# Kernel tuning notes

Measured on AMD Instinct MI355X. Metric: run time of the kernel, lower is better.

## Reference

```python
import jax, jax.numpy as jnp
import numpy as np

B, N, DIM = 4, 1024, 512
H, DH = 8, 64
INNER = H * DH
MLP = 2048
EPS = 1e-5


def layernorm(x, g, b):
    m = x.mean(-1, keepdims=True)
    v = ((x - m) ** 2).mean(-1, keepdims=True)
    return (x - m) / jnp.sqrt(v + EPS) * g + b


def setup_inputs() -> dict:
    key = jax.random.key(0)
    ks = jax.random.split(key, 12)
    s = 0.02
    return {
        "q": jax.random.normal(ks[0], (B, N, DIM), jnp.float32),
        "k": jax.random.normal(ks[1], (B, N, DIM), jnp.float32),
        "v": jax.random.normal(ks[2], (B, N, DIM), jnp.float32),
        "Win": jax.random.normal(ks[3], (INNER, DIM), jnp.float32) * s,
        "Wout": jax.random.normal(ks[4], (DIM, INNER), jnp.float32) * s,
        "bout": jnp.zeros((DIM,), jnp.float32),
        "g1": jnp.ones((DIM,), jnp.float32),
        "b1n": jnp.zeros((DIM,), jnp.float32),
        "g2": jnp.ones((DIM,), jnp.float32),
        "b2n": jnp.zeros((DIM,), jnp.float32),
        "Wup": jax.random.normal(ks[5], (MLP, DIM), jnp.float32) * s,
        "bup": jnp.zeros((MLP,), jnp.float32),
        "Wdn": jax.random.normal(ks[6], (DIM, MLP), jnp.float32) * s,
        "bdn": jnp.zeros((DIM,), jnp.float32),
        "wp_W1": jax.random.normal(ks[7], (DH, 2 * DH), jnp.float32) * s,
        "wp_b1": jnp.zeros((DH,), jnp.float32),
        "wp_g": jnp.ones((DH,), jnp.float32),
        "wp_b": jnp.zeros((DH,), jnp.float32),
        "wp_W2": jax.random.normal(ks[8], (3, DH), jnp.float32) * s,
        "wp_b2": jnp.zeros((3,), jnp.float32),
        "num_heads": H,
        "dim_head": DH,
        "mlp_dim": MLP,
    }


def reference(q, k, v, Win, Wout, bout, g1, b1n, g2, b2n, Wup, bup, Wdn, bdn,
              wp_W1, wp_b1, wp_g, wp_b, wp_W2, wp_b2, num_heads, dim_head, mlp_dim):
    b, n, _ = q.shape

    def split_heads(x):  # [b,n,dim] -> [h,b,n,d]
        f = x @ Win.T
        return f.reshape(b, n, num_heads, dim_head).transpose(2, 0, 1, 3)

    fq = split_heads(layernorm(q, g1, b1n))
    fk = split_heads(layernorm(k, g1, b1n))
    fv = split_heads(layernorm(v, g1, b1n))

    # cosine similarity component
    dots = jnp.einsum('hbnd,hbmd->hbnm', fq, fk)
    nq = jnp.linalg.norm(fq, axis=-1)  # [h,b,n]
    nk = jnp.linalg.norm(fk, axis=-1)  # [h,b,m]
    cosine_sim = dots / (nq[..., :, None] * nk[..., None, :])

    # mean-centered covariance component
    qc = fq - fq.mean(-1, keepdims=True)
    kc = fk - fk.mean(-1, keepdims=True)
    cov_component = jnp.einsum('hbnd,hbmd->hbnm', qc, kc) / dim_head

    # variance outer-product component (torch.var -> unbiased, ddof=1)
    qv = jnp.var(fq, axis=-1, ddof=1)  # [h,b,n]
    kv = jnp.var(fk, axis=-1, ddof=1)  # [h,b,m]
    var_component = qv[..., :, None] * kv[..., None, :] / dim_head

    # dynamic per-head mixing weights
    qg = fq.mean(axis=(1, 2))  # [h,d]
    kg = fk.mean(axis=(1, 2))
    feats = jnp.concatenate([qg, kg], axis=-1)  # [h,2d]
    h1 = jax.nn.relu(layernorm(feats @ wp_W1.T + wp_b1, wp_g, wp_b))
    w = jax.nn.softmax(h1 @ wp_W2.T + wp_b2, axis=-1)  # [h,3]
    cw = w[:, 0][:, None, None, None]
    covw = w[:, 1][:, None, None, None]
    vw = w[:, 2][:, None, None, None]

    scores = cw * cosine_sim + covw * cov_component + vw * var_component
    out = jnp.einsum('hbnm,hbmd->hbnd', scores, fv)
    out = out.transpose(1, 2, 0, 3).reshape(b, n, num_heads * dim_head)
    attn = out @ Wout.T + bout

    q2 = q + attn
    x = layernorm(q2, g2, b2n)
    y = jax.nn.gelu(x @ Wup.T + bup, approximate=False) @ Wdn.T + bdn
    return q2 + y
```

## Files before the change

kernel.cpp:

```cpp
#include <hip/hip_runtime.h>
#include <math.h>

#define EPS 1e-5f
#define ROWS 4096

typedef __attribute__((ext_vector_type(8))) short short8;
typedef __attribute__((ext_vector_type(4))) float floatx4;

__device__ inline short f2bf(float f) {
    unsigned u = __builtin_bit_cast(unsigned, f);
    unsigned r = (u + 0x7fffu + ((u >> 16) & 1u)) >> 16;
    return (short)r;
}
__device__ inline float bf2f(short s) {
    return __builtin_bit_cast(float, (unsigned)(unsigned short)s << 16);
}

__global__ __launch_bounds__(256) void prep(
    const float* __restrict__ q, const float* __restrict__ k,
    const float* __restrict__ v, const float* __restrict__ g,
    const float* __restrict__ bb, short* __restrict__ qkvout,
    const float* __restrict__ w0, const float* __restrict__ w1,
    const float* __restrict__ w2, const float* __restrict__ w3,
    short* __restrict__ o0, short* __restrict__ o1,
    short* __restrict__ o2, short* __restrict__ o3,
    const float* __restrict__ g2, const float* __restrict__ b2n,
    float* __restrict__ Bn, float* __restrict__ Wg,
    float* __restrict__ zero0) {
    int bx = blockIdx.x;
    int t = threadIdx.x;
    if (bx < 3072) {
        int tensor = bx >> 10;
        int xb = bx & 1023;
        const float* x = tensor == 0 ? q : (tensor == 1 ? k : v);
        int row = xb * 4 + (t >> 6);
        int col = (t & 63) * 8;
        const float* xr = x + (size_t)row * 512 + col;
        float4 v0 = *(const float4*)xr;
        float4 v1 = *(const float4*)(xr + 4);
        float s = v0.x + v0.y + v0.z + v0.w + v1.x + v1.y + v1.z + v1.w;
        float sq = v0.x * v0.x + v0.y * v0.y + v0.z * v0.z + v0.w * v0.w +
                   v1.x * v1.x + v1.y * v1.y + v1.z * v1.z + v1.w * v1.w;
#pragma unroll
        for (int off = 32; off; off >>= 1) {
            s += __shfl_xor(s, off);
            sq += __shfl_xor(sq, off);
        }
        float m = s * (1.f / 512.f);
        float rstd = rsqrtf(sq * (1.f / 512.f) - m * m + EPS);
        float4 g0 = *(const float4*)(g + col);
        float4 g1 = *(const float4*)(g + col + 4);
        float4 b0 = *(const float4*)(bb + col);
        float4 b1 = *(const float4*)(bb + col + 4);
        short8 o;
        o[0] = f2bf((v0.x - m) * rstd * g0.x + b0.x);
        o[1] = f2bf((v0.y - m) * rstd * g0.y + b0.y);
        o[2] = f2bf((v0.z - m) * rstd * g0.z + b0.z);
        o[3] = f2bf((v0.w - m) * rstd * g0.w + b0.w);
        o[4] = f2bf((v1.x - m) * rstd * g1.x + b1.x);
        o[5] = f2bf((v1.y - m) * rstd * g1.y + b1.y);
        o[6] = f2bf((v1.z - m) * rstd * g1.z + b1.z);
        o[7] = f2bf((v1.w - m) * rstd * g1.w + b1.w);
        *(short8*)(qkvout + (size_t)(tensor * 4096 + row) * 512 + col) = o;
        return;
    }
    if (bx < 4352) {
        int wb = bx - 3072;
        if (wb >= 256 && wb < 768) {
            int base = wb - 256;
            int idx = base * 2048 + t * 8;
            int n = idx >> 9, c = idx & 511;
            float4 v0 = *(const float4*)(w2 + idx);
            float4 v1 = *(const float4*)(w2 + idx + 4);
            float4 ga = *(const float4*)(g2 + c);
            float4 gb = *(const float4*)(g2 + c + 4);
            float4 ba = *(const float4*)(b2n + c);
            float4 bbv = *(const float4*)(b2n + c + 4);
            short8 o;
            o[0] = f2bf(ga.x * v0.x); o[1] = f2bf(ga.y * v0.y);
            o[2] = f2bf(ga.z * v0.z); o[3] = f2bf(ga.w * v0.w);
            o[4] = f2bf(gb.x * v1.x); o[5] = f2bf(gb.y * v1.y);
            o[6] = f2bf(gb.z * v1.z); o[7] = f2bf(gb.w * v1.w);
            *(short8*)(o2 + idx) = o;
            float bn = ba.x * v0.x + ba.y * v0.y + ba.z * v0.z + ba.w * v0.w +
                       bbv.x * v1.x + bbv.y * v1.y + bbv.z * v1.z + bbv.w * v1.w;
            float wg = ga.x * v0.x + ga.y * v0.y + ga.z * v0.z + ga.w * v0.w +
                       gb.x * v1.x + gb.y * v1.y + gb.z * v1.z + gb.w * v1.w;
#pragma unroll
            for (int off = 32; off; off >>= 1) {
                bn += __shfl_xor(bn, off);
                wg += __shfl_xor(wg, off);
            }
            if ((t & 63) == 0) {
                Bn[n] = bn;
                Wg[n] = wg;
            }
            return;
        }
        const float* src;
        short* dst;
        int base;
        if (wb < 128) { src = w0; dst = o0; base = wb; }
        else if (wb < 256) { src = w1; dst = o1; base = wb - 128; }
        else { src = w3; dst = o3; base = wb - 768; }
        int idx = base * 2048 + t * 8;
        float4 v0 = *(const float4*)(src + idx);
        float4 v1 = *(const float4*)(src + idx + 4);
        short8 o;
        o[0] = f2bf(v0.x); o[1] = f2bf(v0.y); o[2] = f2bf(v0.z); o[3] = f2bf(v0.w);
        o[4] = f2bf(v1.x); o[5] = f2bf(v1.y); o[6] = f2bf(v1.z); o[7] = f2bf(v1.w);
        *(short8*)(dst + idx) = o;
        return;
    }
    int zi = (bx - 4352) * 1024 + t * 4;
    if (zi < 275456) *(float4*)(zero0 + zi) = (float4){0.f, 0.f, 0.f, 0.f};
}

template <int TM, int TN, int EPI, bool OUT_BF16>
__global__ __launch_bounds__(256) void mfma_gemm_nt(
    const short* __restrict__ A, const short* __restrict__ B,
    void* __restrict__ C, int M, int N, int K, int ldk,
    const float* __restrict__ bias, const float* __restrict__ resid,
    short* __restrict__ C2, float* __restrict__ Sb,
    float* __restrict__ qgp, float* __restrict__ kgp) {
    constexpr int FI = TM / 32;
    constexpr int FJ = TN / 32;
    __shared__ short As[2][TM * 32];
    __shared__ short Bs[2][TN * 32];
    int t = threadIdx.x;
    int m0 = blockIdx.y * TM, n0 = blockIdx.x * TN;
    int w = t >> 6, lane = t & 63;
    int wm = (w & 1) * (TM / 2), wn = (w >> 1) * (TN / 2);
    floatx4 acc[FI][FJ];
#pragma unroll
    for (int i = 0; i < FI; ++i)
#pragma unroll
        for (int j = 0; j < FJ; ++j) acc[i][j] = (floatx4){0.f, 0.f, 0.f, 0.f};

    int arow = t >> 2, acol = (t & 3) * 8;
    const short* Ag = A + (size_t)(m0 + arow) * ldk + acol;
    const short* Bg = B + (size_t)(n0 + arow) * ldk + acol;
    int ldsbase = w * 1024;

    auto stage = [&](int k0, int buf) {
#pragma unroll
        for (int u = 0; u < TM / 64; ++u)
            __builtin_amdgcn_global_load_lds(
                (const __attribute__((address_space(1))) void*)(Ag + (size_t)u * 64 * ldk + k0),
                (__attribute__((address_space(3))) void*)((char*)As[buf] + u * 4096 + ldsbase),
                16, 0, 0);
#pragma unroll
        for (int u = 0; u < TN / 64; ++u)
            __builtin_amdgcn_global_load_lds(
                (const __attribute__((address_space(1))) void*)(Bg + (size_t)u * 64 * ldk + k0),
                (__attribute__((address_space(3))) void*)((char*)Bs[buf] + u * 4096 + ldsbase),
                16, 0, 0);
    };

    stage(0, 0);
    __syncthreads();
    int nsteps = K >> 5;
    for (int ks = 0; ks < nsteps; ++ks) {
        int buf = ks & 1;
        if (ks + 1 < nsteps) stage((ks + 1) << 5, buf ^ 1);
        int krow = (lane >> 4) * 8;
        short8 af[FI], bf[FJ];
#pragma unroll
        for (int i = 0; i < FI; ++i)
            af[i] = *(const short8*)&As[buf][(wm + i * 16 + (lane & 15)) * 32 + krow];
#pragma unroll
        for (int j = 0; j < FJ; ++j)
            bf[j] = *(const short8*)&Bs[buf][(wn + j * 16 + (lane & 15)) * 32 + krow];
#pragma unroll
        for (int i = 0; i < FI; ++i)
#pragma unroll
            for (int j = 0; j < FJ; ++j)
                acc[i][j] = __builtin_amdgcn_mfma_f32_16x16x32_bf16(
                    af[i], bf[j], acc[i][j], 0, 0, 0);
        __syncthreads();
    }

    int col = lane & 15, rbase = (lane >> 4) * 4;
    if constexpr (EPI == 5) {
#pragma unroll
        for (int i = 0; i < FI; ++i) {
#pragma unroll
            for (int r = 0; r < 4; ++r) {
                int grow = m0 + wm + i * 16 + rbase + r;
                float s = 0.f, sq = 0.f;
#pragma unroll
                for (int j = 0; j < FJ; ++j) {
                    int gcol = n0 + wn + j * 16 + col;
                    float vv = acc[i][j][r] + bias[gcol] +
                               resid[(size_t)grow * N + gcol];
                    ((float*)C)[(size_t)grow * N + gcol] = vv;
                    C2[(size_t)grow * N + gcol] = f2bf(vv);
                    s += vv;
                    sq += vv * vv;
                }
#pragma unroll
                for (int off = 1; off < 16; off <<= 1) {
                    s += __shfl_xor(s, off);
                    sq += __shfl_xor(sq, off);
                }
                if ((lane & 15) == 0) {
                    atomicAdd(&Sb[grow], s);
                    atomicAdd(&Sb[4096 + grow], sq);
                }
            }
        }
    } else if constexpr (EPI == 4) {
#pragma unroll
        for (int i = 0; i < FI; ++i) {
#pragma unroll
            for (int r = 0; r < 4; ++r) {
                int grow = m0 + wm + i * 16 + rbase + r;
                float m = Sb[grow] * (1.f / 512.f);
                float rstd = rsqrtf(Sb[4096 + grow] * (1.f / 512.f) - m * m + EPS);
                float mrstd = m * rstd;
#pragma unroll
                for (int j = 0; j < FJ; ++j) {
                    int gcol = n0 + wn + j * 16 + col;
                    float vv = rstd * acc[i][j][r] + qgp[gcol] + bias[gcol] -
                               mrstd * kgp[gcol];
                    vv = 0.5f * vv * (1.f + erff(vv * 0.70710678118654752f));
                    ((short*)C)[(size_t)grow * N + gcol] = f2bf(vv);
                }
            }
        }
    } else {
#pragma unroll
        for (int i = 0; i < FI; ++i) {
#pragma unroll
            for (int j = 0; j < FJ; ++j) {
                int gcol = n0 + wn + j * 16 + col;
#pragma unroll
                for (int r = 0; r < 4; ++r) {
                    int grow = m0 + wm + i * 16 + rbase + r;
                    float v = acc[i][j][r];
                    if (EPI == 2) v += bias[gcol] + resid[(size_t)grow * N + gcol];
                    if (OUT_BF16)
                        ((short*)C)[(size_t)grow * N + gcol] = f2bf(v);
                    else
                        ((float*)C)[(size_t)grow * N + gcol] = v;
                }
            }
        }
    }

    if constexpr (EPI == 1) {
        if (m0 < 8192) {
            int tensor = m0 >> 12;
            float* Sbase = Sb + (size_t)tensor * 98304;
            float* dst = tensor ? kgp : qgp;
            int head = (n0 + wn) >> 6;
            int rowbase = (m0 & 4095) + wm;
#pragma unroll
            for (int i = 0; i < FI; ++i) {
#pragma unroll
                for (int r = 0; r < 4; ++r) {
                    float s = 0.f, sq = 0.f;
#pragma unroll
                    for (int j = 0; j < FJ; ++j) {
                        float vv = acc[i][j][r];
                        s += vv;
                        sq += vv * vv;
                    }
#pragma unroll
                    for (int off = 1; off < 16; off <<= 1) {
                        s += __shfl_xor(s, off);
                        sq += __shfl_xor(sq, off);
                    }
                    if ((lane & 15) == 0) {
                        int row = rowbase + i * 16 + rbase + r;
                        int idx = head * ROWS + row;
                        float m = s * (1.f / 64.f);
                        Sbase[idx] = m;
                        Sbase[32768 + idx] = rsqrtf(sq);
                        Sbase[65536 + idx] = (sq - 64.f * m * m) * (1.f / 63.f);
                    }
                }
            }
            float cs[FJ];
#pragma unroll
            for (int j = 0; j < FJ; ++j) {
                float s = 0.f;
#pragma unroll
                for (int i = 0; i < FI; ++i)
#pragma unroll
                    for (int r = 0; r < 4; ++r) s += acc[i][j][r];
                s += __shfl_xor(s, 16);
                s += __shfl_xor(s, 32);
                cs[j] = s;
            }
            if (lane < 16) {
#pragma unroll
                for (int j = 0; j < FJ; ++j)
                    atomicAdd(&dst[head * 64 + j * 16 + lane], cs[j] * (1.f / 4096.f));
            }
        }
    }
}

__global__ __launch_bounds__(256) void kside_fused(
    const short* __restrict__ fkb, const short* __restrict__ fvb,
    const float* __restrict__ rnk, const float* __restrict__ kvv,
    const float* __restrict__ mkm, float* __restrict__ Mnew,
    float* __restrict__ Sv,
    const float* __restrict__ qg, const float* __restrict__ kg,
    const float* __restrict__ W1, const float* __restrict__ b1,
    const float* __restrict__ g, const float* __restrict__ bb,
    const float* __restrict__ W2, const float* __restrict__ b2,
    float* __restrict__ wmix) {
    int t = threadIdx.x;
    if (blockIdx.x == 32) {
        int wv = t >> 6;
        if (wv >= 2) return;
        int h = blockIdx.y * 2 + wv;
        int j = t & 63;
        float acc = 0.f;
        const float* w1r = W1 + j * 128;
        for (int i = 0; i < 64; ++i) acc += qg[h * 64 + i] * w1r[i];
        for (int i = 0; i < 64; ++i) acc += kg[h * 64 + i] * w1r[64 + i];
        acc += b1[j];
        float s = acc, sq = acc * acc;
#pragma unroll
        for (int off = 32; off; off >>= 1) {
            s += __shfl_xor(s, off);
            sq += __shfl_xor(sq, off);
        }
        float m = s * (1.f / 64.f);
        float var = sq * (1.f / 64.f) - m * m;
        float xh = (acc - m) * rsqrtf(var + EPS) * g[j] + bb[j];
        float r = fmaxf(xh, 0.f);
        float l[3];
#pragma unroll
        for (int c = 0; c < 3; ++c) {
            float p = r * W2[c * 64 + j];
#pragma unroll
            for (int off = 32; off; off >>= 1) p += __shfl_xor(p, off);
            l[c] = p + b2[c];
        }
        if (j == 0) {
            float mx = fmaxf(l[0], fmaxf(l[1], l[2]));
            float e0 = expf(l[0] - mx), e1 = expf(l[1] - mx), e2 = expf(l[2] - mx);
            float inv = 1.f / (e0 + e1 + e2);
            wmix[h * 3 + 0] = e0 * inv;
            wmix[h * 3 + 1] = e1 * inv;
            wmix[h * 3 + 2] = e2 * inv;
        }
        return;
    }
    int hb = blockIdx.x, kz = blockIdx.y;
    int h = hb >> 2, b = hb & 3;
    __shared__ __attribute__((aligned(16))) short rawK[32 * 72];
    __shared__ __attribute__((aligned(16))) short rawV[32 * 72];
    __shared__ __attribute__((aligned(16))) short Ktp[64 * 40];
    __shared__ __attribute__((aligned(16))) short Ktr[64 * 40];
    __shared__ __attribute__((aligned(16))) short Vt[64 * 40];
    __shared__ float rs[256], kvs[256], mks[256];
    {
        int sidx = h * ROWS + b * 1024 + kz * 256 + t;
        rs[t] = rnk[sidx];
        kvs[t] = kvv[sidx];
        mks[t] = mkm[sidx];
    }
    int w = t >> 6, lane = t & 63;
    int wm = (w & 1) * 32, wn = (w >> 1) * 32;
    floatx4 accP[2][2], accR[2][2];
#pragma unroll
    for (int i = 0; i < 2; ++i)
#pragma unroll
        for (int j = 0; j < 2; ++j) {
            accP[i][j] = (floatx4){0.f, 0.f, 0.f, 0.f};
            accR[i][j] = (floatx4){0.f, 0.f, 0.f, 0.f};
        }
    float skv_acc = 0.f, smk_acc = 0.f;
    int mrow = t >> 3, dcol = (t & 7) * 8;
    int dT = t >> 2, mg = (t & 3) * 8;
    int krow = (lane >> 4) * 8;

    for (int s = 0; s < 8; ++s) {
        size_t gbase =
            (size_t)(b * 1024 + kz * 256 + s * 32 + mrow) * 512 + h * 64 + dcol;
        short8 k8 = *(const short8*)&fkb[gbase];
        short8 v8 = *(const short8*)&fvb[gbase];
        *(short8*)&rawK[mrow * 72 + dcol] = k8;
        *(short8*)&rawV[mrow * 72 + dcol] = v8;
        __syncthreads();
        short8 okp, okr, ov;
        int mb = s * 32 + mg;
#pragma unroll
        for (int i = 0; i < 8; ++i) {
            short kv_ = rawK[(mg + i) * 72 + dT];
            float kf = bf2f(kv_);
            okp[i] = kv_;
            okr[i] = f2bf(kf * rs[mb + i]);
            short vv_ = rawV[(mg + i) * 72 + dT];
            ov[i] = vv_;
            float vf = bf2f(vv_);
            skv_acc += kvs[mb + i] * vf;
            smk_acc += mks[mb + i] * vf;
        }
        *(short8*)&Ktp[dT * 40 + mg] = okp;
        *(short8*)&Ktr[dT * 40 + mg] = okr;
        *(short8*)&Vt[dT * 40 + mg] = ov;
        __syncthreads();
        short8 afp[2], afr[2], bfv[2];
#pragma unroll
        for (int i = 0; i < 2; ++i) {
            afp[i] = *(const short8*)&Ktp[(wm + i * 16 + (lane & 15)) * 40 + krow];
            afr[i] = *(const short8*)&Ktr[(wm + i * 16 + (lane & 15)) * 40 + krow];
            bfv[i] = *(const short8*)&Vt[(wn + i * 16 + (lane & 15)) * 40 + krow];
        }
#pragma unroll
        for (int i = 0; i < 2; ++i)
#pragma unroll
            for (int j = 0; j < 2; ++j) {
                accP[i][j] = __builtin_amdgcn_mfma_f32_16x16x32_bf16(
                    afp[i], bfv[j], accP[i][j], 0, 0, 0);
                accR[i][j] = __builtin_amdgcn_mfma_f32_16x16x32_bf16(
                    afr[i], bfv[j], accR[i][j], 0, 0, 0);
            }
        __syncthreads();
    }
    int col = lane & 15, rbase = (lane >> 4) * 4;
    float* Cb = Mnew + (size_t)hb * 8192;
#pragma unroll
    for (int i = 0; i < 2; ++i)
#pragma unroll
        for (int j = 0; j < 2; ++j)
#pragma unroll
            for (int r = 0; r < 4; ++r) {
                int ci = (wm + i * 16 + rbase + r) * 64 + wn + j * 16 + col;
                atomicAdd(&Cb[ci], accP[i][j][r]);
                atomicAdd(&Cb[4096 + ci], accR[i][j][r]);
            }
    atomicAdd(&Sv[hb * 128 + dT], skv_acc);
    atomicAdd(&Sv[hb * 128 + 64 + dT], smk_acc);
}

__global__ __launch_bounds__(256) void qside(
    const short* __restrict__ fqb, const float* __restrict__ Mnew,
    const float* __restrict__ Sv, const float* __restrict__ rnq,
    const float* __restrict__ mq, const float* __restrict__ qv,
    const float* __restrict__ wmix, short* __restrict__ attn_out) {
    int ntile = blockIdx.x, hb = blockIdx.y;
    int h = hb >> 2, b = hb & 3;
    __shared__ float M1s[4096], M2s[4096], fqt[4096];
    __shared__ float Skvs[64], Smks[64], rnqs[64], mqs[64], qvs[64];
    int t = threadIdx.x;
    const float* base = Mnew + (size_t)hb * 8192;
#pragma unroll
    for (int u = 0; u < 4; ++u) {
        int idx = t * 4 + u * 1024;
        *(float4*)&M2s[idx] = *(const float4*)&base[idx];
        *(float4*)&M1s[idx] = *(const float4*)&base[4096 + idx];
    }
    int n0 = ntile * 64;
#pragma unroll
    for (int u = 0; u < 2; ++u) {
        int idx = t * 8 + u * 2048;
        int r = idx >> 6, d = idx & 63;
        short8 sv = *(const short8*)&fqb[(size_t)(b * 1024 + n0 + r) * 512 + h * 64 + d];
#pragma unroll
        for (int i = 0; i < 8; ++i) fqt[idx + i] = bf2f(sv[i]);
    }
    if (t < 64) {
        Skvs[t] = Sv[hb * 128 + t];
        Smks[t] = Sv[hb * 128 + 64 + t];
        int sidx = h * ROWS + b * 1024 + n0 + t;
        rnqs[t] = rnq[sidx];
        mqs[t] = mq[sidx];
        qvs[t] = qv[sidx];
    }
    __syncthreads();
    float cw = wmix[h * 3 + 0], covw = wmix[h * 3 + 1], vw = wmix[h * 3 + 2];
    int e = t & 63, rq = t >> 6;
    float a1[16] = {}, a2[16] = {};
    for (int d4 = 0; d4 < 64; d4 += 4) {
        float md1[4], md2[4];
#pragma unroll
        for (int dd = 0; dd < 4; ++dd) {
            md1[dd] = M1s[(d4 + dd) * 64 + e];
            md2[dd] = M2s[(d4 + dd) * 64 + e];
        }
#pragma unroll
        for (int i = 0; i < 16; ++i) {
            float4 f = *(const float4*)&fqt[(rq * 16 + i) * 64 + d4];
            a1[i] += f.x * md1[0] + f.y * md1[1] + f.z * md1[2] + f.w * md1[3];
            a2[i] += f.x * md2[0] + f.y * md2[1] + f.z * md2[2] + f.w * md2[3];
        }
    }
    float c2 = covw * (1.f / 64.f), c3 = vw * (1.f / 64.f);
#pragma unroll
    for (int i = 0; i < 16; ++i) {
        int rr = rq * 16 + i;
        float v = cw * rnqs[rr] * a1[i] + c2 * a2[i] + c3 * qvs[rr] * Skvs[e] -
                  covw * mqs[rr] * Smks[e];
        attn_out[(size_t)(b * 1024 + n0 + rr) * 512 + h * 64 + e] = f2bf(v);
    }
}

extern "C" void kernel_launch(void* const* d_in, const int* in_sizes, int n_in,
                              void* d_out, int out_size, void* d_ws, size_t ws_size,
                              hipStream_t stream) {
    const float* q = (const float*)d_in[0];
    const float* k = (const float*)d_in[1];
    const float* v = (const float*)d_in[2];
    const float* Win = (const float*)d_in[3];
    const float* Wout = (const float*)d_in[4];
    const float* bout = (const float*)d_in[5];
    const float* g1 = (const float*)d_in[6];
    const float* b1n = (const float*)d_in[7];
    const float* g2 = (const float*)d_in[8];
    const float* b2n = (const float*)d_in[9];
    const float* Wup = (const float*)d_in[10];
    const float* bup = (const float*)d_in[11];
    const float* Wdn = (const float*)d_in[12];
    const float* bdn = (const float*)d_in[13];
    const float* wpW1 = (const float*)d_in[14];
    const float* wpb1 = (const float*)d_in[15];
    const float* wpg = (const float*)d_in[16];
    const float* wpb = (const float*)d_in[17];
    const float* wpW2 = (const float*)d_in[18];
    const float* wpb2 = (const float*)d_in[19];
    float* out = (float*)d_out;

    float* wsf = (float*)d_ws;
    short* fqkv = (short*)wsf;
    short* fkb = fqkv + (size_t)4096 * 512;
    short* fvb = fqkv + (size_t)8192 * 512;
    short* qkvln = (short*)(wsf + 3145728);
    short* hmid = (short*)wsf;
    short* attnbf = (short*)(wsf + 4194304);
    short* q2bf = (short*)(wsf + 7340032);
    short* Winbf = (short*)(wsf + 8388608);
    short* Woutbf = (short*)(wsf + 8388608 + 131072);
    short* Wupbf = (short*)(wsf + 8388608 + 262144);
    short* Wdnbf = (short*)(wsf + 8388608 + 262144 + 524288);
    float* S = wsf + 9699328;
    float* qg = S + 196608;
    float* kg = qg + 512;
    float* Mnew = kg + 512;
    float* Sv = Mnew + 262144;
    float* rowstats = Sv + 4096;
    float* wmix = rowstats + 8192;
    float* Bn = wmix + 32;
    float* Wg = Bn + 2048;
    float* mqS = S, *rnqS = S + 32768, *qvS = S + 65536;
    float* mkS = S + 98304, *rnkS = S + 131072, *kvS = S + 163840;

    prep<<<4621, 256, 0, stream>>>(q, k, v, g1, b1n, qkvln,
                                   Win, Wout, Wup, Wdn,
                                   Winbf, Woutbf, Wupbf, Wdnbf,
                                   g2, b2n, Bn, Wg, qg);

    mfma_gemm_nt<64, 128, 1, true><<<dim3(4, 192), 256, 0, stream>>>(
        qkvln, Winbf, fqkv, 12288, 512, 512, 512, nullptr, nullptr, nullptr,
        S, qg, kg);

    kside_fused<<<dim3(33, 4), 256, 0, stream>>>(
        fkb, fvb, rnkS, kvS, mkS, Mnew, Sv,
        qg, kg, wpW1, wpb1, wpg, wpb, wpW2, wpb2, wmix);

    qside<<<dim3(16, 32), 256, 0, stream>>>(fqkv, Mnew, Sv, rnqS, mqS, qvS,
                                            wmix, attnbf);

    mfma_gemm_nt<64, 64, 5, false><<<dim3(8, 64), 256, 0, stream>>>(
        attnbf, Woutbf, out, 4096, 512, 512, 512, bout, q, q2bf,
        rowstats, nullptr, nullptr);

    mfma_gemm_nt<64, 128, 4, true><<<dim3(16, 64), 256, 0, stream>>>(
        q2bf, Wupbf, hmid, 4096, 2048, 512, 512, bup, nullptr, nullptr,
        rowstats, Bn, Wg);

    mfma_gemm_nt<64, 128, 2, false><<<dim3(4, 64), 256, 0, stream>>>(
        hmid, Wdnbf, out, 4096, 512, 2048, 2048, bdn, out, nullptr,
        nullptr, nullptr, nullptr);
}
```

Before: 233.3 us.

## Use bf16 MFMA in qside with transposed M storage; enlarge up-projection tile

The q-side attention contraction moves from scalar fp32 FMAs over shared memory to bf16 MFMA 16x16x32 instructions. To feed it, the k-side atomics now write the M matrices transposed, and qside converts them to bf16 into padded shared tiles. Separately, the MLP up-projection GEMM uses 128-row tiles with half as many blocks. Rounding the M matrices and the fq operand to bf16 adds precision loss, and the larger tile changes occupancy for the up-projection GEMM.

After: 237.7 us. No clear change (+1.9%).

```diff
diff --git a/kernel.cpp b/kernel.cpp
--- a/kernel.cpp
+++ b/kernel.cpp
@@ -432,9 +432,9 @@
         for (int j = 0; j < 2; ++j)
 #pragma unroll
             for (int r = 0; r < 4; ++r) {
-                int ci = (wm + i * 16 + rbase + r) * 64 + wn + j * 16 + col;
-                atomicAdd(&Cb[ci], accP[i][j][r]);
-                atomicAdd(&Cb[4096 + ci], accR[i][j][r]);
+                int ciT = (wn + j * 16 + col) * 64 + (wm + i * 16 + rbase + r);
+                atomicAdd(&Cb[ciT], accP[i][j][r]);
+                atomicAdd(&Cb[4096 + ciT], accR[i][j][r]);
             }
     atomicAdd(&Sv[hb * 128 + dT], skv_acc);
     atomicAdd(&Sv[hb * 128 + 64 + dT], smk_acc);
@@ -447,24 +447,30 @@
     const float* __restrict__ wmix, short* __restrict__ attn_out) {
     int ntile = blockIdx.x, hb = blockIdx.y;
     int h = hb >> 2, b = hb & 3;
-    __shared__ float M1s[4096], M2s[4096], fqt[4096];
+    __shared__ __attribute__((aligned(16))) short M1bf[64 * 72];
+    __shared__ __attribute__((aligned(16))) short M2bf[64 * 72];
+    __shared__ __attribute__((aligned(16))) short fqs[64 * 72];
     __shared__ float Skvs[64], Smks[64], rnqs[64], mqs[64], qvs[64];
     int t = threadIdx.x;
     const float* base = Mnew + (size_t)hb * 8192;
 #pragma unroll
     for (int u = 0; u < 4; ++u) {
         int idx = t * 4 + u * 1024;
-        *(float4*)&M2s[idx] = *(const float4*)&base[idx];
-        *(float4*)&M1s[idx] = *(const float4*)&base[4096 + idx];
+        int e = idx >> 6, d = idx & 63;
+        float4 v2 = *(const float4*)&base[idx];
+        float4 v1 = *(const float4*)&base[4096 + idx];
+        short4 s2 = {f2bf(v2.x), f2bf(v2.y), f2bf(v2.z), f2bf(v2.w)};
+        short4 s1 = {f2bf(v1.x), f2bf(v1.y), f2bf(v1.z), f2bf(v1.w)};
+        *(short4*)&M2bf[e * 72 + d] = s2;
+        *(short4*)&M1bf[e * 72 + d] = s1;
     }
     int n0 = ntile * 64;
 #pragma unroll
     for (int u = 0; u < 2; ++u) {
-        int idx = t * 8 + u * 2048;
-        int r = idx >> 6, d = idx & 63;
-        short8 sv = *(const short8*)&fqb[(size_t)(b * 1024 + n0 + r) * 512 + h * 64 + d];
-#pragma unroll
-        for (int i = 0; i < 8; ++i) fqt[idx + i] = bf2f(sv[i]);
+        int sidx = t * 8 + u * 2048;
+        int r = sidx >> 6, d = sidx & 63;
+        *(short8*)&fqs[r * 72 + d] =
+            *(const short8*)&fqb[(size_t)(b * 1024 + n0 + r) * 512 + h * 64 + d];
     }
     if (t < 64) {
         Skvs[t] = Sv[hb * 128 + t];
@@ -475,31 +481,54 @@
         qvs[t] = qv[sidx];
     }
     __syncthreads();
+    int w = t >> 6, lane = t & 63;
+    int wm = (w & 1) * 32, wn = (w >> 1) * 32;
+    int l15 = lane & 15, krow = (lane >> 4) * 8;
+    floatx4 a1[2][2], a2[2][2];
+#pragma unroll
+    for (int i = 0; i < 2; ++i)
+#pragma unroll
+        for (int j = 0; j < 2; ++j) {
+            a1[i][j] = (floatx4){0.f, 0.f, 0.f, 0.f};
+            a2[i][j] = (floatx4){0.f, 0.f, 0.f, 0.f};
+        }
+#pragma unroll
+    for (int kk = 0; kk < 64; kk += 32) {
+        short8 af[2], b1f[2], b2f[2];
+#pragma unroll
+        for (int i = 0; i < 2; ++i)
+            af[i] = *(const short8*)&fqs[(wm + i * 16 + l15) * 72 + kk + krow];
+#pragma unroll
+        for (int j = 0; j < 2; ++j) {
+            b1f[j] = *(const short8*)&M1bf[(wn + j * 16 + l15) * 72 + kk + krow];
+            b2f[j] = *(const short8*)&M2bf[(wn + j * 16 + l15) * 72 + kk + krow];
+        }
+#pragma unroll
+        for (int i = 0; i < 2; ++i)
+#pragma unroll
+            for (int j = 0; j < 2; ++j) {
+                a1[i][j] = __builtin_amdgcn_mfma_f32_16x16x32_bf16(
+                    af[i], b1f[j], a1[i][j], 0, 0, 0);
+                a2[i][j] = __builtin_amdgcn_mfma_f32_16x16x32_bf16(
+                    af[i], b2f[j], a2[i][j], 0, 0, 0);
+            }
+    }
     float cw = wmix[h * 3 + 0], covw = wmix[h * 3 + 1], vw = wmix[h * 3 + 2];
-    int e = t & 63, rq = t >> 6;
-    float a1[16] = {}, a2[16] = {};
-    for (int d4 = 0; d4 < 64; d4 += 4) {
-        float md1[4], md2[4];
-#pragma unroll
-        for (int dd = 0; dd < 4; ++dd) {
-            md1[dd] = M1s[(d4 + dd) * 64 + e];
-            md2[dd] = M2s[(d4 + dd) * 64 + e];
-        }
-#pragma unroll
-        for (int i = 0; i < 16; ++i) {
-            float4 f = *(const float4*)&fqt[(rq * 16 + i) * 64 + d4];
-            a1[i] += f.x * md1[0] + f.y * md1[1] + f.z * md1[2] + f.w * md1[3];
-            a2[i] += f.x * md2[0] + f.y * md2[1] + f.z * md2[2] + f.w * md2[3];
-        }
-    }
     float c2 = covw * (1.f / 64.f), c3 = vw * (1.f / 64.f);
-#pragma unroll
-    for (int i = 0; i < 16; ++i) {
-        int rr = rq * 16 + i;
-        float v = cw * rnqs[rr] * a1[i] + c2 * a2[i] + c3 * qvs[rr] * Skvs[e] -
-                  covw * mqs[rr] * Smks[e];
-        attn_out[(size_t)(b * 1024 + n0 + rr) * 512 + h * 64 + e] = f2bf(v);
-    }
+    int col = lane & 15, rb = (lane >> 4) * 4;
+#pragma unroll
+    for (int i = 0; i < 2; ++i)
+#pragma unroll
+        for (int j = 0; j < 2; ++j)
+#pragma unroll
+            for (int r = 0; r < 4; ++r) {
+                int row = wm + i * 16 + rb + r;
+                int e = wn + j * 16 + col;
+                float v = cw * rnqs[row] * a1[i][j][r] + c2 * a2[i][j][r] +
+                          c3 * qvs[row] * Skvs[e] - covw * mqs[row] * Smks[e];
+                attn_out[(size_t)(b * 1024 + n0 + row) * 512 + h * 64 + e] =
+                    f2bf(v);
+            }
 }
 
 extern "C" void kernel_launch(void* const* d_in, const int* in_sizes, int n_in,
@@ -571,7 +600,7 @@
         attnbf, Woutbf, out, 4096, 512, 512, 512, bout, q, q2bf,
         rowstats, nullptr, nullptr);
 
-    mfma_gemm_nt<64, 128, 4, true><<<dim3(16, 64), 256, 0, stream>>>(
+    mfma_gemm_nt<128, 128, 4, true><<<dim3(16, 32), 256, 0, stream>>>(
         q2bf, Wupbf, hmid, 4096, 2048, 512, 512, bup, nullptr, nullptr,
         rowstats, Bn, Wg);
 
```
